# Optimization experiments

Hardware: AMD Instinct MI355X
Metric: run time of the kernel (lower is better)

Reference implementation:

```python
import jax, jax.numpy as jnp
import numpy as np

DIM = 128; DSTATE = 8; DCONV = 4; DTRANK = 8
B = 2; T = 48; H = 16; W = 16
EPS = 1e-5

def _ln(x, w, b):
    mu = jnp.mean(x, -1, keepdims=True)
    var = jnp.mean(jnp.square(x - mu), -1, keepdims=True)
    return (x - mu) * jax.lax.rsqrt(var + EPS) * w + b

def _causal_dwconv(x, w, b):
    # x: [B,L,D], w: [D,K] depthwise, causal padding K-1 on the left
    xt = jnp.transpose(x, (0, 2, 1))  # [B,D,L]
    out = jax.lax.conv_general_dilated(
        xt, w[:, None, :], (1,), [(w.shape[-1] - 1, 0)],
        dimension_numbers=('NCH', 'OIH', 'NCH'),
        feature_group_count=x.shape[-1])
    return jnp.transpose(out + b[:, None], (0, 2, 1))

def _selective_scan(u, dt, A, Bc, Cc, Dp):
    # u, dt: [B,L,D]; A: [D,N]; Bc, Cc: [B,L,N]; Dp: [D]
    dA = jnp.exp(dt[..., None] * A)                          # [B,L,D,N]
    dBx = dt[..., None] * Bc[:, :, None, :] * u[..., None]   # [B,L,D,N]
    def combine(c1, c2):
        a1, b1 = c1; a2, b2 = c2
        return a1 * a2, a2 * b1 + b2
    _, hs = jax.lax.associative_scan(combine, (dA, dBx), axis=1)
    return jnp.einsum('bldn,bln->bld', hs, Cc) + u * Dp

def _bimamba(xn, in_w, conv_w, conv_b, xp_w, dt_w, dt_b, A_log, Dp, out_w):
    # xn: [B,L,DIM]; direction-stacked params have leading axis 2 (fwd/bwd)
    xz = xn @ in_w.T                      # [B,L,2*DIM]
    xh, z = jnp.split(xz, 2, axis=-1)
    acc = 0.0
    for d in range(2):
        xi = xh if d == 0 else xh[:, ::-1]
        zi = z if d == 0 else z[:, ::-1]
        xc = jax.nn.silu(_causal_dwconv(xi, conv_w[d], conv_b[d]))
        proj = xc @ xp_w[d].T             # [B,L,DTRANK+2*DSTATE]
        dtr, Bc, Cc = jnp.split(proj, [DTRANK, DTRANK + DSTATE], axis=-1)
        dt = jax.nn.softplus(dtr @ dt_w[d].T + dt_b[d])
        A = -jnp.exp(A_log[d])
        y = _selective_scan(xc, dt, A, Bc, Cc, Dp[d]) * jax.nn.silu(zi)
        acc = acc + (y if d == 0 else y[:, ::-1])
    return acc @ out_w.T

def setup_inputs():
    key = jax.random.key(0)
    ks = jax.random.split(key, 10)
    s = 0.1
    return {
        "x": jax.random.normal(ks[0], (B, DIM, T, H, W), jnp.float32),
        "norm1_w": jnp.ones((DIM,), jnp.float32),
        "norm1_b": jnp.zeros((DIM,), jnp.float32),
        "norm2_w": jnp.ones((DIM,), jnp.float32),
        "norm2_b": jnp.zeros((DIM,), jnp.float32),
        "subln_w": jnp.ones((DIM,), jnp.float32),
        "subln_b": jnp.zeros((DIM,), jnp.float32),
        "lambda_q": jax.random.normal(ks[1], (DIM,), jnp.float32) * s,
        "in_proj_w": jax.random.normal(ks[2], (2, 2 * DIM, DIM), jnp.float32) * s,
        "conv_w": jax.random.normal(ks[3], (2, 2, DIM, DCONV), jnp.float32) * s,
        "conv_b": jax.random.normal(ks[4], (2, 2, DIM), jnp.float32) * s,
        "x_proj_w": jax.random.normal(ks[5], (2, 2, DTRANK + 2 * DSTATE, DIM), jnp.float32) * s,
        "dt_proj_w": jax.random.normal(ks[6], (2, 2, DIM, DTRANK), jnp.float32) * s,
        "dt_proj_b": jax.random.normal(ks[7], (2, 2, DIM), jnp.float32) * s,
        "A_log": jnp.broadcast_to(jnp.log(jnp.arange(1, DSTATE + 1, dtype=jnp.float32)), (2, 2, DIM, DSTATE)) + 0.0,
        "D": jnp.ones((2, 2, DIM), jnp.float32),
        "out_proj_w": jax.random.normal(ks[8], (2, DIM, DIM), jnp.float32) * s,
    }

def reference(x, norm1_w, norm1_b, norm2_w, norm2_b, subln_w, subln_b,
              lambda_q, in_proj_w, conv_w, conv_b, x_proj_w,
              dt_proj_w, dt_proj_b, A_log, D, out_proj_w):
    Bsz, C = x.shape[0], x.shape[1]
    Tt, Hh, Ww = x.shape[2], x.shape[3], x.shape[4]
    L = Tt * Hh * Ww
    x_flat = jnp.transpose(x.reshape(Bsz, C, L), (0, 2, 1))  # [B,L,C]
    x_norm = _ln(x_flat, norm1_w, norm1_b)
    y1 = _bimamba(x_norm, in_proj_w[0], conv_w[0], conv_b[0], x_proj_w[0],
                  dt_proj_w[0], dt_proj_b[0], A_log[0], D[0], out_proj_w[0])
    y2 = _bimamba(x_norm, in_proj_w[1], conv_w[1], conv_b[1], x_proj_w[1],
                  dt_proj_w[1], dt_proj_b[1], A_log[1], D[1], out_proj_w[1])
    lam = jax.nn.sigmoid(jnp.sum(lambda_q))
    attn = _ln(y1 - lam * y2, subln_w, subln_b)
    out = _ln(x_flat + attn, norm2_w, norm2_b)
    return jnp.transpose(out, (0, 2, 1)).reshape(Bsz, C, Tt, Hh, Ww)
```

## Files before the change

### kernel.cpp

```cpp
#include <hip/hip_runtime.h>
#include <math.h>

#define DIMC 128
#define LSEQ 12288
#define NB 2
#define BLR 24576
#define EPSV 1e-5f
#define NCH 384
#define LC 32
#define KP 132
#define FBP 20

typedef __bf16 bf16x8 __attribute__((ext_vector_type(8)));
typedef __attribute__((ext_vector_type(4))) float f4_t;

__device__ __forceinline__ float sigf(float x){ return 1.f/(1.f+__expf(-x)); }
__device__ __forceinline__ float softplusf(float x){
    return fmaxf(x,0.f) + __logf(1.f + __expf(-fabsf(x)));
}
__device__ __forceinline__ float bf2f(unsigned short u){
    union { unsigned int i; float f; } v; v.i = ((unsigned int)u) << 16; return v.f;
}
__device__ __forceinline__ unsigned short f2bf(float f){
    union { float f; unsigned int i; } v; v.f = f;
    unsigned int b = v.i + 0x7FFFu + ((v.i >> 16) & 1u);
    return (unsigned short)(b >> 16);
}
__device__ __forceinline__ bf16x8 ld_frag8(const unsigned short* p){
    union { uint2 u[2]; bf16x8 v; } r;
    r.u[0] = *(const uint2*)(p);
    r.u[1] = *(const uint2*)(p+4);
    return r.v;
}
__device__ __forceinline__ bf16x8 ld_frag16g(const unsigned short* p){
    union { uint4 u; bf16x8 v; } r; r.u = *(const uint4*)p; return r.v;
}

template<bool FAST>
__device__ __forceinline__ void comp_a8(float dtv, const float* Av, float* a){
    if (FAST){
        float e1 = __expf(dtv*Av[0]);
        float e2 = e1*e1, e4 = e2*e2;
        a[0]=e1; a[1]=e2; a[2]=e2*e1; a[3]=e4;
        a[4]=e4*e1; a[5]=e4*e2; a[6]=a[5]*e1; a[7]=e4*e4;
    } else {
        #pragma unroll
        for (int n = 0; n < 8; n++) a[n] = __expf(dtv*Av[n]);
    }
}

__global__ __launch_bounds__(128) void k_wall(const float* __restrict__ dtw, const float* __restrict__ xpw,
                       const float* __restrict__ lq, const float* __restrict__ wi, const float* __restrict__ ow,
                       unsigned short* __restrict__ wallb, float* __restrict__ lam,
                       unsigned short* __restrict__ wib, unsigned short* __restrict__ owb){
    int b = blockIdx.x, k = threadIdx.x;
    if (b < 576){
        int inst = b & 3, j = b >> 2;
        const float* xp = xpw + (size_t)inst*24*128;
        float v;
        if (j < 128){
            const float* dw = dtw + (size_t)inst*128*8 + (size_t)j*8;
            v = 0.f;
            #pragma unroll
            for (int r = 0; r < 8; r++) v += dw[r]*xp[r*128 + k];
        } else {
            v = xp[(8 + (j-128))*128 + k];
        }
        wallb[((size_t)inst*144 + j)*128 + k] = f2bf(v);
        if (b == 0 && k < 64){
            float s = lq[k] + lq[k+64];
            for (int m = 32; m; m >>= 1) s += __shfl_xor(s, m);
            if (k == 0) *lam = 1.f/(1.f+__expf(-s));
        }
    } else {
        int idx = ((b-576)*128 + k)*4;
        const float* src; unsigned short* dst; int off;
        if (idx < 65536){ src = wi;  dst = wib; off = idx; }
        else            { src = ow;  dst = owb; off = idx - 65536; }
        float4 v = *(const float4*)&src[off];
        ushort4 o; o.x=f2bf(v.x); o.y=f2bf(v.y); o.z=f2bf(v.z); o.w=f2bf(v.w);
        *(ushort4*)&dst[off] = o;
    }
}

__global__ __launch_bounds__(256,4) void k_inproj(const float* __restrict__ x,
    const float* __restrict__ w1, const float* __restrict__ b1,
    const unsigned short* __restrict__ wib, unsigned short* __restrict__ xz)
{
    __shared__ __align__(16) unsigned short As[64*KP];
    __shared__ float red1[256], red2[256];
    __shared__ float stt[128];
    const int row0 = blockIdx.x * 64;
    const int bb = blockIdx.x / 192;
    const int l0 = (blockIdx.x % 192) * 64;
    const int j0 = blockIdx.y * 128;
    const int tid = threadIdx.x;
    const int li = tid & 63, cg = tid >> 6;
    const float* xb = x + (size_t)bb*DIMC*LSEQ + l0 + li;
    {
        float s = 0.f, s2 = 0.f;
        #pragma unroll
        for (int p = 0; p < 32; p++){
            float v = xb[(size_t)(p*4 + cg)*LSEQ];
            s += v; s2 += v*v;
        }
        red1[cg*64 + li] = s; red2[cg*64 + li] = s2;
    }
    __syncthreads();
    if (tid < 64){
        float ss = 0.f, ss2 = 0.f;
        #pragma unroll
        for (int g = 0; g < 4; g++){ ss += red1[g*64 + tid]; ss2 += red2[g*64 + tid]; }
        float mu = ss*(1.f/128.f);
        float var = ss2*(1.f/128.f) - mu*mu;
        stt[tid*2] = mu; stt[tid*2+1] = rsqrtf(var + EPSV);
    }
    __syncthreads();
    {
        float mu = stt[li*2], rs = stt[li*2+1];
        #pragma unroll
        for (int p = 0; p < 32; p++){
            int c = p*4 + cg;
            float v = (xb[(size_t)c*LSEQ] - mu)*rs*w1[c] + b1[c];
            As[li*KP + c] = f2bf(v);
        }
    }
    __syncthreads();
    const int lane = tid & 63, w = tid >> 6;
    const int m15 = lane & 15, q = lane >> 4;
    const unsigned short* wb = wib + ((size_t)j0 + m15)*DIMC + q*8;
    bf16x8 bc[8], bn[8];
    #pragma unroll
    for (int nt = 0; nt < 8; nt++) bc[nt] = ld_frag16g(wb + nt*2048);
    f4_t zf = {0.f,0.f,0.f,0.f};
    f4_t acc[8];
    #pragma unroll
    for (int j = 0; j < 8; j++) acc[j] = zf;
    #pragma unroll
    for (int ks = 0; ks < 4; ks++){
        if (ks < 3){
            #pragma unroll
            for (int nt = 0; nt < 8; nt++) bn[nt] = ld_frag16g(wb + nt*2048 + (ks+1)*32);
        }
        bf16x8 a0 = ld_frag8(&As[(w*16 + m15)*KP + ks*32 + q*8]);
        #pragma unroll
        for (int nt = 0; nt < 8; nt++)
            acc[nt] = __builtin_amdgcn_mfma_f32_16x16x32_bf16(a0, bc[nt], acc[nt], 0,0,0);
        #pragma unroll
        for (int nt = 0; nt < 8; nt++) bc[nt] = bn[nt];
    }
    __syncthreads();
    unsigned short* ep = As;
    #pragma unroll
    for (int nt = 0; nt < 8; nt++){
        int row = w*16 + q*4;
        int col = nt*16 + m15;
        #pragma unroll
        for (int i = 0; i < 4; i++)
            ep[(row+i)*KP + col] = f2bf(acc[nt][i]);
    }
    __syncthreads();
    #pragma unroll
    for (int p = 0; p < 4; p++){
        int idx = p*256 + tid; int li2 = idx >> 4; int g = (idx & 15)*8;
        uint2 u0 = *(const uint2*)&ep[li2*KP + g];
        uint2 u1 = *(const uint2*)&ep[li2*KP + g + 4];
        uint4 o; o.x=u0.x; o.y=u0.y; o.z=u1.x; o.w=u1.y;
        *(uint4*)&xz[(size_t)(row0+li2)*512 + j0 + g] = o;
    }
}

template<bool FAST>
__device__ __forceinline__ void fscan(const unsigned short* __restrict__ As,
    const unsigned short* __restrict__ Ep, const float* __restrict__ fbuf,
    const float* Av, int ch, int d, int dim, float* Ac, float* Bc)
{
    float dts = 0.f;
    #pragma unroll 8
    for (int s = 0; s < LC; s++){
        int r = ch*32 + (d ? 31-s : s);
        float dtv = bf2f(Ep[r*KP + dim]);
        float uv  = bf2f(As[r*KP + dim]);
        float4 b0 = *(const float4*)&fbuf[r*FBP];
        float4 b1 = *(const float4*)&fbuf[r*FBP + 4];
        float bv[8] = {b0.x,b0.y,b0.z,b0.w,b1.x,b1.y,b1.z,b1.w};
        float du = dtv*uv;
        float a[8];
        comp_a8<FAST>(dtv, Av, a);
        #pragma unroll
        for (int n = 0; n < 8; n++)
            Bc[n] = a[n]*Bc[n] + du*bv[n];
        dts += dtv;
    }
    comp_a8<FAST>(dts, Av, Ac);
}

__global__ __launch_bounds__(256,4) void k_xproj(const unsigned short* __restrict__ xz,
    const unsigned short* __restrict__ wallb, const float* __restrict__ dtb,
    const float* __restrict__ alog, const float* __restrict__ cw, const float* __restrict__ cbv,
    unsigned short* __restrict__ xc, unsigned short* __restrict__ dty,
    float* __restrict__ bcb, float* __restrict__ st)
{
    __shared__ __align__(16) unsigned short As[64*KP];
    __shared__ __align__(16) unsigned short Zb[67*KP];
    __shared__ __align__(16) float fbuf[64*FBP];
    const int row0 = blockIdx.x * 64;
    const int ib   = blockIdx.y;
    const int inst = ib >> 1;
    const int bb   = ib & 1;
    const int m    = inst >> 1;
    const int d    = inst & 1;
    const int tid = threadIdx.x;
    const size_t abase = (size_t)ib * LSEQ * DIMC;
    const int lane = tid & 63, w = tid >> 6;
    const int m15 = lane & 15, q = lane >> 4;
    const unsigned short* wb = wallb + ((size_t)inst*144 + m15)*DIMC + q*8;
    bf16x8 bc[9], bn[9];
    #pragma unroll
    for (int nt = 0; nt < 9; nt++) bc[nt] = ld_frag16g(wb + nt*2048);
    const int start = row0 - (d ? 0 : 3);
    for (int idx = tid; idx < 67*16; idx += 256){
        int r = idx >> 4, cq = idx & 15;
        int l = start + r;
        uint4 v = make_uint4(0,0,0,0);
        if (l >= 0 && l < LSEQ)
            v = *(const uint4*)&xz[((size_t)(bb*LSEQ + l))*512 + m*256 + cq*8];
        *(uint4*)&Zb[r*KP + cq*8] = v;
    }
    __syncthreads();
    {
        const int dimi = tid & 127, lg = tid >> 7;
        float wk[4];
        #pragma unroll
        for (int k = 0; k < 4; k++){
            int kk = d ? 3-k : k;
            wk[k] = cw[((size_t)inst*DIMC + dimi)*4 + kk];
        }
        const float bsv = cbv[inst*DIMC + dimi];
        const int base = lg*32;
        float t0 = bf2f(Zb[(base  )*KP + dimi]);
        float t1 = bf2f(Zb[(base+1)*KP + dimi]);
        float t2 = bf2f(Zb[(base+2)*KP + dimi]);
        for (int p = 0; p < 32; p++){
            int li = base + p;
            float t3 = bf2f(Zb[(li+3)*KP + dimi]);
            float v = bsv + wk[0]*t0 + wk[1]*t1 + wk[2]*t2 + wk[3]*t3;
            v = v * sigf(v);
            As[li*KP + dimi] = f2bf(v);
            t0 = t1; t1 = t2; t2 = t3;
        }
    }
    __syncthreads();
    #pragma unroll
    for (int p = 0; p < 4; p++){
        int idx = p*256 + tid; int li = idx >> 4; int g = (idx & 15)*8;
        uint2 u0 = *(const uint2*)&As[li*KP + g];
        uint2 u1 = *(const uint2*)&As[li*KP + g + 4];
        uint4 o; o.x=u0.x; o.y=u0.y; o.z=u1.x; o.w=u1.y;
        *(uint4*)&xc[abase + (size_t)(row0+li)*DIMC + g] = o;
    }
    f4_t zf = {0.f,0.f,0.f,0.f};
    f4_t acc[9];
    #pragma unroll
    for (int j = 0; j < 9; j++) acc[j] = zf;
    #pragma unroll
    for (int ks = 0; ks < 4; ks++){
        if (ks < 3){
            #pragma unroll
            for (int nt = 0; nt < 9; nt++) bn[nt] = ld_frag16g(wb + nt*2048 + (ks+1)*32);
        }
        bf16x8 a0 = ld_frag8(&As[(w*16 + m15)*KP + ks*32 + q*8]);
        #pragma unroll
        for (int nt = 0; nt < 9; nt++)
            acc[nt] = __builtin_amdgcn_mfma_f32_16x16x32_bf16(a0, bc[nt], acc[nt], 0,0,0);
        #pragma unroll
        for (int nt = 0; nt < 9; nt++) bc[nt] = bn[nt];
    }
    unsigned short* Ep = Zb;
    {
        int row = w*16 + q*4;
        #pragma unroll
        for (int i = 0; i < 4; i++)
            fbuf[(row+i)*FBP + m15] = acc[8][i];
    }
    #pragma unroll
    for (int nt = 0; nt < 8; nt++){
        int col = nt*16 + m15;
        float bias = dtb[inst*DIMC + col];
        int row = w*16 + q*4;
        #pragma unroll
        for (int i = 0; i < 4; i++)
            Ep[(row+i)*KP + col] = f2bf(softplusf(acc[nt][i] + bias));
    }
    __syncthreads();
    {
        int row = tid >> 2, j = (tid & 3)*4;
        float4 v = { fbuf[row*FBP + j], fbuf[row*FBP + j + 1],
                     fbuf[row*FBP + j + 2], fbuf[row*FBP + j + 3] };
        *(float4*)&bcb[((size_t)ib*LSEQ + row0 + row)*16 + j] = v;
    }
    #pragma unroll
    for (int p = 0; p < 4; p++){
        int idx = p*256 + tid; int li = idx >> 4; int g = (idx & 15)*8;
        uint2 u0 = *(const uint2*)&Ep[li*KP + g];
        uint2 u1 = *(const uint2*)&Ep[li*KP + g + 4];
        uint4 o; o.x=u0.x; o.y=u0.y; o.z=u1.x; o.w=u1.y;
        *(uint4*)&dty[abase + (size_t)(row0+li)*DIMC + g] = o;
    }
    const int ch  = tid >> 7;
    const int dim = tid & 127;
    const int bc2 = row0 >> 5;
    const int c   = d ? (NCH-1 - bc2 - ch) : (bc2 + ch);
    float Av[8];
    #pragma unroll
    for (int n = 0; n < 8; n++)
        Av[n] = -__expf(alog[((size_t)inst*DIMC + dim)*8 + n]);
    bool fast = true;
    #pragma unroll
    for (int n = 1; n < 8; n++)
        fast = fast && (fabsf(Av[n] - (float)(n+1)*Av[0]) <= 1e-5f*fabsf(Av[n]));
    float Ac[8], Bc[8];
    #pragma unroll
    for (int n = 0; n < 8; n++){ Ac[n] = 1.f; Bc[n] = 0.f; }
    if (fast) fscan<true >(As, Ep, fbuf, Av, ch, d, dim, Ac, Bc);
    else      fscan<false>(As, Ep, fbuf, Av, ch, d, dim, Ac, Bc);
    float* so = st + (((size_t)ib*NCH + c)*DIMC + dim)*16;
    float4 s0 = {Ac[0],Ac[1],Ac[2],Ac[3]};
    float4 s1 = {Ac[4],Ac[5],Ac[6],Ac[7]};
    float4 s2 = {Bc[0],Bc[1],Bc[2],Bc[3]};
    float4 s3 = {Bc[4],Bc[5],Bc[6],Bc[7]};
    *(float4*)&so[0]  = s0;
    *(float4*)&so[4]  = s1;
    *(float4*)&so[8]  = s2;
    *(float4*)&so[12] = s3;
}

__global__ __launch_bounds__(512) void k_scan2(float* __restrict__ st){
    const int ib   = blockIdx.x >> 7;
    const int dim  = blockIdx.x & 127;
    const int n    = threadIdx.x >> 6;
    const int lane = threadIdx.x & 63;
    const size_t cstride = (size_t)DIMC*16;
    const size_t base = ((size_t)ib*NCH*DIMC + dim)*16 + n;
    float a[6], b[6];
    float Al = 1.f, Bl = 0.f;
    #pragma unroll
    for (int j = 0; j < 6; j++){
        size_t o = base + (size_t)(lane*6 + j)*cstride;
        float A  = st[o];
        float Bv = st[o + 8];
        a[j] = A; b[j] = Bv;
        Bl = A*Bl + Bv;
        Al *= A;
    }
    #pragma unroll
    for (int off = 1; off < 64; off <<= 1){
        float Ao = __shfl_up(Al, off, 64);
        float Bo = __shfl_up(Bl, off, 64);
        if (lane >= off){
            Bl = Al*Bo + Bl;
            Al = Al*Ao;
        }
    }
    float h = __shfl_up(Bl, 1, 64);
    if (lane == 0) h = 0.f;
    #pragma unroll
    for (int j = 0; j < 6; j++){
        size_t o = base + (size_t)(lane*6 + j)*cstride;
        st[o] = h;
        h = a[j]*h + b[j];
    }
}

template<bool FAST>
__device__ __forceinline__ void scan3_body(unsigned short* __restrict__ dty,
    const unsigned short* __restrict__ sdt, const unsigned short* __restrict__ sxc,
    const unsigned short* __restrict__ sz, const float* __restrict__ sbc,
    const float* Av, float Dv, float* h,
    size_t rbase, size_t lbase, int d, int tid)
{
    #pragma unroll 8
    for (int s = 0; s < LC; s++){
        int r = d ? 31-s : s;
        float dtv = bf2f(sdt[r*128 + tid]);
        float uv  = bf2f(sxc[r*128 + tid]);
        float zv  = bf2f(sz [r*128 + tid]);
        float4 bA = *(const float4*)&sbc[r*16];
        float4 bB = *(const float4*)&sbc[r*16 + 4];
        float4 cA = *(const float4*)&sbc[r*16 + 8];
        float4 cB = *(const float4*)&sbc[r*16 + 12];
        float bv[8] = {bA.x,bA.y,bA.z,bA.w,bB.x,bB.y,bB.z,bB.w};
        float cv[8] = {cA.x,cA.y,cA.z,cA.w,cB.x,cB.y,cB.z,cB.w};
        float du = dtv*uv;
        float y = uv*Dv;
        float a[8];
        comp_a8<FAST>(dtv, Av, a);
        #pragma unroll
        for (int n = 0; n < 8; n++){
            h[n] = a[n]*h[n] + du*bv[n];
            y += h[n]*cv[n];
        }
        y *= zv * sigf(zv);
        dty[rbase + (lbase + r)*DIMC + tid] = f2bf(y);
    }
}

__global__ __launch_bounds__(128) void k_scan3(unsigned short* __restrict__ dty,
    const unsigned short* __restrict__ xc, const float* __restrict__ bcb,
    const unsigned short* __restrict__ xz, const float* __restrict__ st,
    const float* __restrict__ alog, const float* __restrict__ dvec)
{
    __shared__ __align__(16) unsigned short sdt[32*128];
    __shared__ __align__(16) unsigned short sxc[32*128];
    __shared__ __align__(16) unsigned short sz [32*128];
    __shared__ __align__(16) float sbc[32*16];
    const int ib = blockIdx.x & 7;
    const int c  = blockIdx.x >> 3;
    const int inst = ib >> 1, bb = ib & 1;
    const int m = inst >> 1, d = inst & 1;
    const int tid = threadIdx.x;
    const size_t rbase = (size_t)ib*LSEQ*DIMC;
    const size_t zbase = (size_t)bb*LSEQ*512 + m*256 + 128;
    const size_t lbase = d ? (size_t)(LSEQ - 32 - c*32) : (size_t)(c*32);
    #pragma unroll
    for (int p = 0; p < 4; p++){
        int idx = p*128 + tid;
        int r = idx >> 4, g = (idx & 15)*8;
        size_t go = rbase + (lbase + r)*DIMC + g;
        *(uint4*)&sdt[r*128 + g] = *(const uint4*)&dty[go];
        *(uint4*)&sxc[r*128 + g] = *(const uint4*)&xc[go];
        *(uint4*)&sz [r*128 + g] = *(const uint4*)&xz[zbase + (lbase + r)*512 + g];
    }
    {
        int r = tid >> 2, j = (tid & 3)*4;
        *(float4*)&sbc[r*16 + j] = *(const float4*)&bcb[((size_t)ib*LSEQ + lbase + r)*16 + j];
    }
    float Av[8];
    #pragma unroll
    for (int n = 0; n < 8; n++)
        Av[n] = -__expf(alog[((size_t)inst*DIMC + tid)*8 + n]);
    bool fast = true;
    #pragma unroll
    for (int n = 1; n < 8; n++)
        fast = fast && (fabsf(Av[n] - (float)(n+1)*Av[0]) <= 1e-5f*fabsf(Av[n]));
    const float Dv = dvec[inst*DIMC + tid];
    float h[8];
    const float* hp = st + (((size_t)ib*NCH + c)*DIMC + tid)*16;
    #pragma unroll
    for (int n = 0; n < 8; n++) h[n] = hp[n];
    __syncthreads();
    if (fast) scan3_body<true >(dty, sdt, sxc, sz, sbc, Av, Dv, h, rbase, lbase, d, tid);
    else      scan3_body<false>(dty, sdt, sxc, sz, sbc, Av, Dv, h, rbase, lbase, d, tid);
}

__global__ __launch_bounds__(256,4) void k_final(const unsigned short* __restrict__ y,
    const unsigned short* __restrict__ owb, const float* __restrict__ x, const float* __restrict__ lamp,
    const float* __restrict__ sw, const float* __restrict__ sb,
    const float* __restrict__ n2w, const float* __restrict__ n2b, float* __restrict__ outp)
{
    __shared__ __align__(16) char smem[36352];
    unsigned short* Ast = (unsigned short*)smem;
    float* yt            = (float*)smem;
    float* red1          = (float*)(smem + 33792);
    float* red2          = (float*)(smem + 34816);
    float* stt           = (float*)(smem + 35840);
    const int bb = blockIdx.y;
    const int l0 = blockIdx.x * 64;
    const int tid = threadIdx.x;
    const float lam = *lamp;
    #pragma unroll
    for (int p = 0; p < 8; p++){
        int idx = p*256 + tid; int mm = idx >> 10; int li = (idx >> 4) & 63; int g = (idx & 15)*8;
        uint4 vf = *(const uint4*)&y[(((size_t)(mm*2+0)*NB + bb)*LSEQ + l0 + li)*DIMC + g];
        uint4 vb = *(const uint4*)&y[(((size_t)(mm*2+1)*NB + bb)*LSEQ + l0 + li)*DIMC + g];
        const unsigned short* uf = (const unsigned short*)&vf;
        const unsigned short* ub = (const unsigned short*)&vb;
        unsigned short o[8];
        #pragma unroll
        for (int j = 0; j < 8; j++) o[j] = f2bf(bf2f(uf[j]) + bf2f(ub[j]));
        *(uint2*)&Ast[(mm*64 + li)*KP + g]     = *(uint2*)&o[0];
        *(uint2*)&Ast[(mm*64 + li)*KP + g + 4] = *(uint2*)&o[4];
    }
    __syncthreads();
    const int lane = tid & 63, w = tid >> 6;
    const int m15 = lane & 15, q = lane >> 4;
    f4_t zf = {0.f,0.f,0.f,0.f};
    f4_t acc[2][8];
    #pragma unroll
    for (int i = 0; i < 2; i++)
        #pragma unroll
        for (int j = 0; j < 8; j++) acc[i][j] = zf;
    #pragma unroll
    for (int ks = 0; ks < 4; ks++){
        int k0 = ks*32 + q*8;
        bf16x8 a0 = ld_frag8(&Ast[(       w*16 + m15)*KP + k0]);
        bf16x8 a1 = ld_frag8(&Ast[(64   + w*16 + m15)*KP + k0]);
        #pragma unroll
        for (int nt = 0; nt < 8; nt++){
            bf16x8 b0 = ld_frag16g(&owb[((size_t)0*DIMC + nt*16 + m15)*DIMC + k0]);
            bf16x8 b1 = ld_frag16g(&owb[((size_t)1*DIMC + nt*16 + m15)*DIMC + k0]);
            acc[0][nt] = __builtin_amdgcn_mfma_f32_16x16x32_bf16(a0, b0, acc[0][nt], 0,0,0);
            acc[1][nt] = __builtin_amdgcn_mfma_f32_16x16x32_bf16(a1, b1, acc[1][nt], 0,0,0);
        }
    }
    __syncthreads();
    #pragma unroll
    for (int nt = 0; nt < 8; nt++){
        int row = w*16 + q*4;
        int col = nt*16 + m15;
        #pragma unroll
        for (int i = 0; i < 4; i++)
            yt[(row+i)*129 + col] = acc[0][nt][i] - lam*acc[1][nt][i];
    }
    __syncthreads();
    const int r = tid & 63, g = tid >> 6;
    float s = 0.f, s2 = 0.f;
    #pragma unroll
    for (int k = 0; k < 32; k++){ float v = yt[r*129 + g*32 + k]; s += v; s2 += v*v; }
    red1[g*64 + r] = s; red2[g*64 + r] = s2;
    __syncthreads();
    if (tid < 64){
        float ss = 0.f, ss2 = 0.f;
        #pragma unroll
        for (int gg = 0; gg < 4; gg++){ ss += red1[gg*64 + tid]; ss2 += red2[gg*64 + tid]; }
        float mu = ss*(1.f/128.f);
        float var = ss2*(1.f/128.f) - mu*mu;
        stt[tid*2] = mu; stt[tid*2+1] = rsqrtf(var + EPSV);
    }
    __syncthreads();
    float mu1 = stt[r*2], rs1 = stt[r*2+1];
    s = 0.f; s2 = 0.f;
    #pragma unroll
    for (int k = 0; k < 32; k++){
        int c = g*32 + k;
        float v = (yt[r*129+c] - mu1)*rs1*sw[c] + sb[c]
                + x[(size_t)bb*DIMC*LSEQ + (size_t)c*LSEQ + l0 + r];
        yt[r*129+c] = v;
        s += v; s2 += v*v;
    }
    __syncthreads();
    red1[g*64 + r] = s; red2[g*64 + r] = s2;
    __syncthreads();
    if (tid < 64){
        float ss = 0.f, ss2 = 0.f;
        #pragma unroll
        for (int gg = 0; gg < 4; gg++){ ss += red1[gg*64 + tid]; ss2 += red2[gg*64 + tid]; }
        float mu = ss*(1.f/128.f);
        float var = ss2*(1.f/128.f) - mu*mu;
        stt[tid*2] = mu; stt[tid*2+1] = rsqrtf(var + EPSV);
    }
    __syncthreads();
    float mu2 = stt[r*2], rs2 = stt[r*2+1];
    #pragma unroll
    for (int k = 0; k < 32; k++){
        int c = g*32 + k;
        float o = (yt[r*129+c] - mu2)*rs2*n2w[c] + n2b[c];
        outp[(size_t)bb*DIMC*LSEQ + (size_t)c*LSEQ + l0 + r] = o;
    }
}

extern "C" void kernel_launch(void* const* d_in, const int* in_sizes, int n_in,
                              void* d_out, int out_size, void* d_ws, size_t ws_size,
                              hipStream_t stream)
{
    const float* x    = (const float*)d_in[0];
    const float* n1w  = (const float*)d_in[1];
    const float* n1b  = (const float*)d_in[2];
    const float* n2w  = (const float*)d_in[3];
    const float* n2b  = (const float*)d_in[4];
    const float* slw  = (const float*)d_in[5];
    const float* slb  = (const float*)d_in[6];
    const float* lq   = (const float*)d_in[7];
    const float* wi   = (const float*)d_in[8];
    const float* cw   = (const float*)d_in[9];
    const float* cb   = (const float*)d_in[10];
    const float* xpw  = (const float*)d_in[11];
    const float* dtw  = (const float*)d_in[12];
    const float* dtb  = (const float*)d_in[13];
    const float* alog = (const float*)d_in[14];
    const float* dvec = (const float*)d_in[15];
    const float* ow   = (const float*)d_in[16];

    float* ws = (float*)d_ws;
    unsigned short* xz    = (unsigned short*)(ws + 1572864);
    unsigned short* xc    = (unsigned short*)(ws + 7864320);
    unsigned short* dty   = (unsigned short*)(ws + 14155776);
    float*          bcb   = ws + 20447232;
    float*          st1   = ws + 22020096;
    unsigned short* wallb = (unsigned short*)(ws + 28311552);
    unsigned short* wib   = (unsigned short*)(ws + 28348416);
    unsigned short* owb   = (unsigned short*)(ws + 28381184);
    float*          lam   = ws + 28397568;

    k_wall  <<<768, 128, 0, stream>>>(dtw, xpw, lq, wi, ow, wallb, lam, wib, owb);
    k_inproj<<<dim3(384, 4), 256, 0, stream>>>(x, n1w, n1b, wib, xz);
    k_xproj <<<dim3(192, 8), 256, 0, stream>>>(xz, wallb, dtb, alog, cw, cb, xc, dty, bcb, st1);
    k_scan2 <<<1024, 512, 0, stream>>>(st1);
    k_scan3 <<<8*NCH, 128, 0, stream>>>(dty, xc, bcb, xz, st1, alog, dvec);
    k_final <<<dim3(192, 2), 256, 0, stream>>>(dty, owb, x, lam, slw, slb, n2w, n2b, (float*)d_out);
}
```

Measured before the change: 269.6 us.

## Precompute LayerNorm stats once in k_wall and software-pipeline scan loads

LayerNorm mean and rstd for each row are now computed once by extra blocks in the weight-conversion kernel and stored in the workspace. k_inproj no longer recomputes them in each of its 4 column blocks, which removes a redundant pass over x and two block barriers. Separately, the scan loops in fscan and scan3_body prefetch the next step's LDS operands before computing the current step, to hide LDS latency. This costs extra registers and another global read of the stats.

After: 276.4 us. +2.5%, slower.

```diff
diff --git a/kernel.cpp b/kernel.cpp
--- a/kernel.cpp
+++ b/kernel.cpp
@@ -51,8 +51,11 @@
 
 __global__ __launch_bounds__(128) void k_wall(const float* __restrict__ dtw, const float* __restrict__ xpw,
                        const float* __restrict__ lq, const float* __restrict__ wi, const float* __restrict__ ow,
+                       const float* __restrict__ x,
                        unsigned short* __restrict__ wallb, float* __restrict__ lam,
-                       unsigned short* __restrict__ wib, unsigned short* __restrict__ owb){
+                       unsigned short* __restrict__ wib, unsigned short* __restrict__ owb,
+                       float* __restrict__ stt_g){
+    __shared__ float red[256];
     int b = blockIdx.x, k = threadIdx.x;
     if (b < 576){
         int inst = b & 3, j = b >> 2;
@@ -72,7 +75,7 @@
             for (int m = 32; m; m >>= 1) s += __shfl_xor(s, m);
             if (k == 0) *lam = 1.f/(1.f+__expf(-s));
         }
-    } else {
+    } else if (b < 768){
         int idx = ((b-576)*128 + k)*4;
         const float* src; unsigned short* dst; int off;
         if (idx < 65536){ src = wi;  dst = wib; off = idx; }
@@ -80,16 +83,36 @@
         float4 v = *(const float4*)&src[off];
         ushort4 o; o.x=f2bf(v.x); o.y=f2bf(v.y); o.z=f2bf(v.z); o.w=f2bf(v.w);
         *(ushort4*)&dst[off] = o;
+    } else {
+        int t = b - 768;
+        int bb = t / 192, l0 = (t % 192) * 64;
+        int li = k & 63, cg = k >> 6;
+        const float* xb = x + (size_t)bb*DIMC*LSEQ + l0 + li;
+        float s = 0.f, s2 = 0.f;
+        #pragma unroll
+        for (int p = 0; p < 64; p++){
+            float v = xb[(size_t)(p*2 + cg)*LSEQ];
+            s += v; s2 += v*v;
+        }
+        red[cg*64 + li] = s; red[128 + cg*64 + li] = s2;
+        __syncthreads();
+        if (k < 64){
+            float ss  = red[k]       + red[64 + k];
+            float ss2 = red[128 + k] + red[192 + k];
+            float mu = ss*(1.f/128.f);
+            float var = ss2*(1.f/128.f) - mu*mu;
+            size_t o = (size_t)(bb*LSEQ + l0 + k)*2;
+            stt_g[o]   = mu;
+            stt_g[o+1] = rsqrtf(var + EPSV);
+        }
     }
 }
 
 __global__ __launch_bounds__(256,4) void k_inproj(const float* __restrict__ x,
-    const float* __restrict__ w1, const float* __restrict__ b1,
+    const float* __restrict__ w1, const float* __restrict__ b1, const float* __restrict__ stt_g,
     const unsigned short* __restrict__ wib, unsigned short* __restrict__ xz)
 {
     __shared__ __align__(16) unsigned short As[64*KP];
-    __shared__ float red1[256], red2[256];
-    __shared__ float stt[128];
     const int row0 = blockIdx.x * 64;
     const int bb = blockIdx.x / 192;
     const int l0 = (blockIdx.x % 192) * 64;
@@ -98,26 +121,8 @@
     const int li = tid & 63, cg = tid >> 6;
     const float* xb = x + (size_t)bb*DIMC*LSEQ + l0 + li;
     {
-        float s = 0.f, s2 = 0.f;
-        #pragma unroll
-        for (int p = 0; p < 32; p++){
-            float v = xb[(size_t)(p*4 + cg)*LSEQ];
-            s += v; s2 += v*v;
-        }
-        red1[cg*64 + li] = s; red2[cg*64 + li] = s2;
-    }
-    __syncthreads();
-    if (tid < 64){
-        float ss = 0.f, ss2 = 0.f;
-        #pragma unroll
-        for (int g = 0; g < 4; g++){ ss += red1[g*64 + tid]; ss2 += red2[g*64 + tid]; }
-        float mu = ss*(1.f/128.f);
-        float var = ss2*(1.f/128.f) - mu*mu;
-        stt[tid*2] = mu; stt[tid*2+1] = rsqrtf(var + EPSV);
-    }
-    __syncthreads();
-    {
-        float mu = stt[li*2], rs = stt[li*2+1];
+        float2 st2 = *(const float2*)&stt_g[(size_t)(row0 + li)*2];
+        float mu = st2.x, rs = st2.y;
         #pragma unroll
         for (int p = 0; p < 32; p++){
             int c = p*4 + cg;
@@ -176,21 +181,30 @@
     const float* Av, int ch, int d, int dim, float* Ac, float* Bc)
 {
     float dts = 0.f;
+    int r0 = ch*32 + (d ? 31 : 0);
+    float dtv = bf2f(Ep[r0*KP + dim]);
+    float uv  = bf2f(As[r0*KP + dim]);
+    float4 b0 = *(const float4*)&fbuf[r0*FBP];
+    float4 b1 = *(const float4*)&fbuf[r0*FBP + 4];
     #pragma unroll 8
     for (int s = 0; s < LC; s++){
-        int r = ch*32 + (d ? 31-s : s);
-        float dtv = bf2f(Ep[r*KP + dim]);
-        float uv  = bf2f(As[r*KP + dim]);
-        float4 b0 = *(const float4*)&fbuf[r*FBP];
-        float4 b1 = *(const float4*)&fbuf[r*FBP + 4];
-        float bv[8] = {b0.x,b0.y,b0.z,b0.w,b1.x,b1.y,b1.z,b1.w};
-        float du = dtv*uv;
+        float dtc = dtv, uvc = uv;
+        float4 b0c = b0, b1c = b1;
+        if (s+1 < LC){
+            int rn = ch*32 + (d ? 31-(s+1) : (s+1));
+            dtv = bf2f(Ep[rn*KP + dim]);
+            uv  = bf2f(As[rn*KP + dim]);
+            b0  = *(const float4*)&fbuf[rn*FBP];
+            b1  = *(const float4*)&fbuf[rn*FBP + 4];
+        }
+        float bv[8] = {b0c.x,b0c.y,b0c.z,b0c.w,b1c.x,b1c.y,b1c.z,b1c.w};
+        float du = dtc*uvc;
         float a[8];
-        comp_a8<FAST>(dtv, Av, a);
+        comp_a8<FAST>(dtc, Av, a);
         #pragma unroll
         for (int n = 0; n < 8; n++)
             Bc[n] = a[n]*Bc[n] + du*bv[n];
-        dts += dtv;
+        dts += dtc;
     }
     comp_a8<FAST>(dts, Av, Ac);
 }
@@ -379,29 +393,44 @@
     const float* Av, float Dv, float* h,
     size_t rbase, size_t lbase, int d, int tid)
 {
+    int r0 = d ? 31 : 0;
+    float dtv = bf2f(sdt[r0*128 + tid]);
+    float uv  = bf2f(sxc[r0*128 + tid]);
+    float zv  = bf2f(sz [r0*128 + tid]);
+    float4 bA = *(const float4*)&sbc[r0*16];
+    float4 bB = *(const float4*)&sbc[r0*16 + 4];
+    float4 cA = *(const float4*)&sbc[r0*16 + 8];
+    float4 cB = *(const float4*)&sbc[r0*16 + 12];
+    int rc = r0;
     #pragma unroll 8
     for (int s = 0; s < LC; s++){
-        int r = d ? 31-s : s;
-        float dtv = bf2f(sdt[r*128 + tid]);
-        float uv  = bf2f(sxc[r*128 + tid]);
-        float zv  = bf2f(sz [r*128 + tid]);
-        float4 bA = *(const float4*)&sbc[r*16];
-        float4 bB = *(const float4*)&sbc[r*16 + 4];
-        float4 cA = *(const float4*)&sbc[r*16 + 8];
-        float4 cB = *(const float4*)&sbc[r*16 + 12];
-        float bv[8] = {bA.x,bA.y,bA.z,bA.w,bB.x,bB.y,bB.z,bB.w};
-        float cv[8] = {cA.x,cA.y,cA.z,cA.w,cB.x,cB.y,cB.z,cB.w};
-        float du = dtv*uv;
-        float y = uv*Dv;
+        float dtc = dtv, uvc = uv, zvc = zv;
+        float4 bAc = bA, bBc = bB, cAc = cA, cBc = cB;
+        int rr = rc;
+        if (s+1 < LC){
+            int rn = d ? 31-(s+1) : (s+1);
+            dtv = bf2f(sdt[rn*128 + tid]);
+            uv  = bf2f(sxc[rn*128 + tid]);
+            zv  = bf2f(sz [rn*128 + tid]);
+            bA  = *(const float4*)&sbc[rn*16];
+            bB  = *(const float4*)&sbc[rn*16 + 4];
+            cA  = *(const float4*)&sbc[rn*16 + 8];
+            cB  = *(const float4*)&sbc[rn*16 + 12];
+            rc = rn;
+        }
+        float bv[8] = {bAc.x,bAc.y,bAc.z,bAc.w,bBc.x,bBc.y,bBc.z,bBc.w};
+        float cv[8] = {cAc.x,cAc.y,cAc.z,cAc.w,cBc.x,cBc.y,cBc.z,cBc.w};
+        float du = dtc*uvc;
+        float y = uvc*Dv;
         float a[8];
-        comp_a8<FAST>(dtv, Av, a);
+        comp_a8<FAST>(dtc, Av, a);
         #pragma unroll
         for (int n = 0; n < 8; n++){
             h[n] = a[n]*h[n] + du*bv[n];
             y += h[n]*cv[n];
         }
-        y *= zv * sigf(zv);
-        dty[rbase + (lbase + r)*DIMC + tid] = f2bf(y);
+        y *= zvc * sigf(zvc);
+        dty[rbase + (lbase + rr)*DIMC + tid] = f2bf(y);
     }
 }
 
@@ -582,6 +611,7 @@
     const float* ow   = (const float*)d_in[16];
 
     float* ws = (float*)d_ws;
+    float*          sttg  = ws;
     unsigned short* xz    = (unsigned short*)(ws + 1572864);
     unsigned short* xc    = (unsigned short*)(ws + 7864320);
     unsigned short* dty   = (unsigned short*)(ws + 14155776);
@@ -592,8 +622,8 @@
     unsigned short* owb   = (unsigned short*)(ws + 28381184);
     float*          lam   = ws + 28397568;
 
-    k_wall  <<<768, 128, 0, stream>>>(dtw, xpw, lq, wi, ow, wallb, lam, wib, owb);
-    k_inproj<<<dim3(384, 4), 256, 0, stream>>>(x, n1w, n1b, wib, xz);
+    k_wall  <<<1152, 128, 0, stream>>>(dtw, xpw, lq, wi, ow, x, wallb, lam, wib, owb, sttg);
+    k_inproj<<<dim3(384, 4), 256, 0, stream>>>(x, n1w, n1b, sttg, wib, xz);
     k_xproj <<<dim3(192, 8), 256, 0, stream>>>(xz, wallb, dtb, alog, cw, cb, xc, dty, bcb, st1);
     k_scan2 <<<1024, 512, 0, stream>>>(st1);
     k_scan3 <<<8*NCH, 128, 0, stream>>>(dty, xc, bcb, xz, st1, alog, dvec);
```
